# Performance work log

Hardware: AMD Instinct MI355X
Metric: run time of the kernel (lower is better)

## Reference

```python
import jax, jax.numpy as jnp
import numpy as np

H = 512      # rnn_cell_dim
CE = 128     # char_embedding
WE = 256     # word_embedding
NC = 256     # num_chars
NW = 100000  # num_words
U = 2048     # unique word forms in batch
TC = 16      # max chars per word
B = 256      # batch (sentences)
TW = 64      # max sentence length


def setup_inputs() -> dict:
    key = jax.random.key(0)
    ks = jax.random.split(key, 16)
    s = 0.05
    n = jax.random.normal
    return {
        "charseqs": jax.random.randint(ks[0], (U, TC), 0, NC),
        "charseq_lens": jax.random.randint(ks[1], (U,), 1, TC + 1),
        "charseq_ids": jax.random.randint(ks[2], (B, TW), 0, U),
        "word_ids": jax.random.randint(ks[3], (B, TW), 0, NW),
        "sentence_lens": jax.random.randint(ks[4], (B,), 1, TW + 1),
        "char_emb": n(ks[5], (NC, CE)) * s,
        "word_emb": n(ks[6], (NW, WE)) * s,
        # char GRU (shared between fw/bw, as in the TF1 code which passes the same cell)
        "Wg_c": n(ks[7], (CE + H, 2 * H)) * s,
        "bg_c": jnp.ones((2 * H,)),   # TF GRUCell gate bias init = 1.0
        "Wc_c": n(ks[8], (CE + H, H)) * s,
        "bc_c": jnp.zeros((H,)),
        # word GRU: input = concat(char bi-state 2H, word_emb WE)
        "Wg_w": n(ks[9], (2 * H + WE + H, 2 * H)) * s,
        "bg_w": jnp.ones((2 * H,)),
        "Wc_w": n(ks[10], (2 * H + WE + H, H)) * s,
        "bc_w": jnp.zeros((H,)),
        # fc head: 2H -> 64 -> 2
        "W1": n(ks[11], (2 * H, 64)) * s,
        "b1": jnp.zeros((64,)),
        "W2": n(ks[12], (64, 2)) * s,
        "b2": jnp.zeros((2,)),
    }


def _gru_final(xs, lengths, Wg, bg, Wc, bc):
    # xs: [N, T, D]; returns final state [N, H], frozen past each sequence length
    N, T, _ = xs.shape
    Hd = Wc.shape[1]
    mask = jnp.arange(T)[None, :] < lengths[:, None]  # [N, T]

    def step(h, xm):
        x, m = xm
        gates = jax.nn.sigmoid(jnp.concatenate([x, h], axis=-1) @ Wg + bg)
        r, u = jnp.split(gates, 2, axis=-1)
        c = jnp.tanh(jnp.concatenate([x, r * h], axis=-1) @ Wc + bc)
        hn = u * h + (1.0 - u) * c
        return jnp.where(m[:, None], hn, h), None

    h0 = jnp.zeros((N, Hd), xs.dtype)
    hT, _ = jax.lax.scan(step, h0, (jnp.swapaxes(xs, 0, 1), mask.T))
    return hT


def _bi_gru_final(xs, lengths, Wg, bg, Wc, bc):
    # bidirectional final states with shared weights; bw = run on per-row reversed seq
    T = xs.shape[1]
    fw = _gru_final(xs, lengths, Wg, bg, Wc, bc)
    ridx = jnp.clip(lengths[:, None] - 1 - jnp.arange(T)[None, :], 0, T - 1)  # [N, T]
    rev = jnp.take_along_axis(xs, ridx[:, :, None], axis=1)
    bw = _gru_final(rev, lengths, Wg, bg, Wc, bc)
    return jnp.concatenate([fw, bw], axis=-1)  # [N, 2H]


def reference(charseqs, charseq_lens, charseq_ids, word_ids, sentence_lens,
              char_emb, word_emb, Wg_c, bg_c, Wc_c, bc_c,
              Wg_w, bg_w, Wc_w, bc_w, W1, b1, W2, b2):
    # char embeddings + char bi-GRU over unique word forms
    input_chars = char_emb[charseqs]                                   # [U, TC, CE]
    char_states = _bi_gru_final(input_chars, charseq_lens, Wg_c, bg_c, Wc_c, bc_c)  # [U, 2H]
    input_char_words = char_states[charseq_ids]                        # [B, TW, 2H]
    # word embeddings (dropout off: inference)
    input_words = word_emb[word_ids]                                   # [B, TW, WE]
    inputs = jnp.concatenate([input_char_words, input_words], axis=2)  # [B, TW, 2H+WE]
    states = _bi_gru_final(inputs, sentence_lens, Wg_w, bg_w, Wc_w, bc_w)  # [B, 2H]
    hidden = jax.nn.leaky_relu(states @ W1 + b1, 0.2)  # tf.nn.leaky_relu alpha=0.2
    logits = hidden @ W2 + b2                                          # [B, 2]
    return logits
```

## Files before the change

### kernel.cpp

```cpp
#include <hip/hip_runtime.h>
#include <math.h>


#define TILE 64
#define BKK 16

typedef __attribute__((ext_vector_type(8))) short bshort8;
typedef __attribute__((ext_vector_type(4))) float f32x4;

enum AMode { A_PLAIN = 0, A_CHARSTATE = 1, A_RH = 2, A_GATHER = 3 };
enum EMode { E_BIAS = 0, E_GATE_CHAR = 1, E_CAND_CHAR = 2, E_XW = 3 };

struct GemmArgs {
  int M, N, K;
  const float* A; int lda;
  const float* G; int ldg;
  const int*   arows;
  const float* B;
  const float* bias;
  const float* XT; int ldxt;
  const int*   seqs;
  const int*   lens;
  int t, T;
  const int*   cidx;
  const float* Hin;
  float* Cout; int ldc;
};

__device__ __forceinline__ float sigmoidf_(float x) { return 1.0f / (1.0f + expf(-x)); }
__device__ __forceinline__ float bf2f_(unsigned short u) {
  return __uint_as_float((unsigned int)u << 16);
}
__device__ __forceinline__ unsigned short f2bf_(float f) {
  const unsigned int u = __float_as_uint(f);
  return (unsigned short)((u + 0x7FFFu + ((u >> 16) & 1u)) >> 16);
}

template<int AM, int EM>
__global__ __launch_bounds__(256) void gemm_k(GemmArgs p) {
  __shared__ float As[BKK][TILE];
  __shared__ float Bs[BKK][TILE];
  const int tid = threadIdx.x;
  const int tx = tid & 15, ty = tid >> 4;
  const int m0 = blockIdx.y * TILE, n0 = blockIdx.x * TILE;
  const int la_r = tid >> 2, la_k = (tid & 3) << 2;
  const int lb_k = tid >> 4, lb_n = (tid & 15) << 2;

  float acc[4][4] = {};
  int arow = 0;
  if constexpr (AM == A_GATHER) arow = p.arows[m0 + la_r];

  for (int k0 = 0; k0 < p.K; k0 += BKK) {
    float4 av;
    const int m = m0 + la_r;
    const int k = k0 + la_k;
    if constexpr (AM == A_PLAIN) {
      av = *reinterpret_cast<const float4*>(p.A + (size_t)m * p.lda + k);
    } else if constexpr (AM == A_CHARSTATE) {
      const float* ap = (k < 512) ? (p.A + (size_t)m * 512 + k)
                                  : (p.A + (size_t)(2048 + m) * 512 + (k - 512));
      av = *reinterpret_cast<const float4*>(ap);
    } else {
      av = *reinterpret_cast<const float4*>(p.A + (size_t)arow * p.lda + k);
    }
    As[la_k + 0][la_r] = av.x;
    As[la_k + 1][la_r] = av.y;
    As[la_k + 2][la_r] = av.z;
    As[la_k + 3][la_r] = av.w;
    float4 bv = *reinterpret_cast<const float4*>(p.B + (size_t)(k0 + lb_k) * p.N + n0 + lb_n);
    *reinterpret_cast<float4*>(&Bs[lb_k][lb_n]) = bv;
    __syncthreads();
#pragma unroll
    for (int kk = 0; kk < BKK; ++kk) {
      float4 a = *reinterpret_cast<const float4*>(&As[kk][ty << 2]);
      float4 b = *reinterpret_cast<const float4*>(&Bs[kk][tx << 2]);
      acc[0][0] += a.x * b.x; acc[0][1] += a.x * b.y; acc[0][2] += a.x * b.z; acc[0][3] += a.x * b.w;
      acc[1][0] += a.y * b.x; acc[1][1] += a.y * b.y; acc[1][2] += a.y * b.z; acc[1][3] += a.y * b.w;
      acc[2][0] += a.z * b.x; acc[2][1] += a.z * b.y; acc[2][2] += a.z * b.z; acc[2][3] += a.z * b.w;
      acc[3][0] += a.w * b.x; acc[3][1] += a.w * b.y; acc[3][2] += a.w * b.z; acc[3][3] += a.w * b.w;
    }
    __syncthreads();
  }

  const int rbase = m0 + (ty << 2);
  const int cbase = n0 + (tx << 2);
#pragma unroll
  for (int i = 0; i < 4; ++i) {
    const int row = rbase + i;
    if constexpr (EM == E_BIAS) {
#pragma unroll
      for (int j = 0; j < 4; ++j) {
        const int col = cbase + j;
        p.Cout[(size_t)row * p.ldc + col] = acc[i][j] + p.bias[col];
      }
    } else {
      const int cs = p.cidx[row];
      const float* xrow = p.XT + (size_t)cs * p.ldxt;
#pragma unroll
      for (int j = 0; j < 4; ++j) {
        const int col = cbase + j;
        p.Cout[(size_t)row * p.ldc + col] = acc[i][j] + xrow[col];
      }
    }
  }
}

__global__ __launch_bounds__(256) void wconv_k(const float* __restrict__ src,
                                               unsigned short* __restrict__ dst,
                                               int n) {
  const int i = blockIdx.x * 256 + threadIdx.x;
  if (i < n) dst[i] = f2bf_(src[i]);
}

template<int BN, int EM>
__global__ __launch_bounds__(256) void cgemm_mfma(
    const float* __restrict__ Ain,
    const float* __restrict__ G,
    const unsigned short* __restrict__ Bw,
    int ldb,
    const float* __restrict__ XT,
    const int* __restrict__ seqs,
    const int* __restrict__ lens,
    int t,
    const float* __restrict__ Hin,
    float* __restrict__ Cout, int ldc) {
  __shared__ unsigned short As[64][40];
  __shared__ unsigned short Bs[BN][40];
  __shared__ int xo_s[64];
  __shared__ int msk_s[64];

  const int tid = threadIdx.x;
  const int m0 = blockIdx.y * 64;
  const int n0 = blockIdx.x * BN;

  if (tid < 64) {
    const int grow = m0 + tid;
    const int us = grow & 2047;
    const bool dir = grow >= 2048;
    const int len = lens[us];
    int pos = dir ? (len - 1 - t) : t;
    pos = pos < 0 ? 0 : (pos > 15 ? 15 : pos);
    const int ch = seqs[us * 16 + pos];
    xo_s[tid] = ch * ((EM == 0) ? 1024 : 512);
    msk_s[tid] = (t < len) ? 1 : 0;
  }

  const int wid = tid >> 6, lane = tid & 63;
  const int lr = lane & 15, lk = (lane >> 4) << 3;
  constexpr int NI = BN / 64;
  const int c0w = wid * (BN / 4);

  f32x4 acc[4][NI];
#pragma unroll
  for (int mi = 0; mi < 4; ++mi)
#pragma unroll
    for (int ni = 0; ni < NI; ++ni) acc[mi][ni] = (f32x4){0.f, 0.f, 0.f, 0.f};

  const int arow = tid >> 2;
  const int akoff = (tid & 3) << 3;

  for (int k0 = 0; k0 < 512; k0 += 32) {
    {
      const float* ap = Ain + (size_t)(m0 + arow) * 512 + k0 + akoff;
      float4 a0 = *reinterpret_cast<const float4*>(ap);
      float4 a1 = *reinterpret_cast<const float4*>(ap + 4);
      if constexpr (EM == 1) {
        const float* gp = G + (size_t)(m0 + arow) * 1024 + k0 + akoff;
        float4 g0 = *reinterpret_cast<const float4*>(gp);
        float4 g1 = *reinterpret_cast<const float4*>(gp + 4);
        a0.x *= g0.x; a0.y *= g0.y; a0.z *= g0.z; a0.w *= g0.w;
        a1.x *= g1.x; a1.y *= g1.y; a1.z *= g1.z; a1.w *= g1.w;
      }
      bshort8 av;
      av[0] = (short)f2bf_(a0.x); av[1] = (short)f2bf_(a0.y);
      av[2] = (short)f2bf_(a0.z); av[3] = (short)f2bf_(a0.w);
      av[4] = (short)f2bf_(a1.x); av[5] = (short)f2bf_(a1.y);
      av[6] = (short)f2bf_(a1.z); av[7] = (short)f2bf_(a1.w);
      *reinterpret_cast<bshort8*>(&As[arow][akoff]) = av;
    }
    if (BN == 128 || tid < 128) {
      const int bc0 = (BN == 128) ? ((tid & 31) << 2) : ((tid & 15) << 2);
      const int bk0 = (BN == 128) ? ((tid >> 5) << 2) : ((tid >> 4) << 2);
      ushort4 b0 = *reinterpret_cast<const ushort4*>(Bw + (size_t)(k0 + bk0 + 0) * ldb + n0 + bc0);
      ushort4 b1 = *reinterpret_cast<const ushort4*>(Bw + (size_t)(k0 + bk0 + 1) * ldb + n0 + bc0);
      ushort4 b2 = *reinterpret_cast<const ushort4*>(Bw + (size_t)(k0 + bk0 + 2) * ldb + n0 + bc0);
      ushort4 b3 = *reinterpret_cast<const ushort4*>(Bw + (size_t)(k0 + bk0 + 3) * ldb + n0 + bc0);
      ushort4 w;
      w.x = b0.x; w.y = b1.x; w.z = b2.x; w.w = b3.x;
      *reinterpret_cast<ushort4*>(&Bs[bc0 + 0][bk0]) = w;
      w.x = b0.y; w.y = b1.y; w.z = b2.y; w.w = b3.y;
      *reinterpret_cast<ushort4*>(&Bs[bc0 + 1][bk0]) = w;
      w.x = b0.z; w.y = b1.z; w.z = b2.z; w.w = b3.z;
      *reinterpret_cast<ushort4*>(&Bs[bc0 + 2][bk0]) = w;
      w.x = b0.w; w.y = b1.w; w.z = b2.w; w.w = b3.w;
      *reinterpret_cast<ushort4*>(&Bs[bc0 + 3][bk0]) = w;
    }
    __syncthreads();

    bshort8 af[4];
#pragma unroll
    for (int mi = 0; mi < 4; ++mi)
      af[mi] = *reinterpret_cast<const bshort8*>(&As[mi * 16 + lr][lk]);
#pragma unroll
    for (int ni = 0; ni < NI; ++ni) {
      const bshort8 bf = *reinterpret_cast<const bshort8*>(&Bs[c0w + ni * 16 + lr][lk]);
#pragma unroll
      for (int mi = 0; mi < 4; ++mi)
        acc[mi][ni] = __builtin_amdgcn_mfma_f32_16x16x32_bf16(af[mi], bf, acc[mi][ni], 0, 0, 0);
    }
    __syncthreads();
  }

  const int rq = lane >> 4;
#pragma unroll
  for (int mi = 0; mi < 4; ++mi) {
#pragma unroll
    for (int ni = 0; ni < NI; ++ni) {
#pragma unroll
      for (int reg = 0; reg < 4; ++reg) {
        const int lrow = mi * 16 + rq * 4 + reg;
        const int grow = m0 + lrow;
        const int col = n0 + c0w + ni * 16 + lr;
        const float v = acc[mi][ni][reg];
        if constexpr (EM == 0) {
          Cout[(size_t)grow * ldc + col] = sigmoidf_(v + XT[xo_s[lrow] + col]);
        } else {
          const float cv = tanhf(v + XT[xo_s[lrow] + col]);
          const float u = G[(size_t)grow * 1024 + 512 + col];
          const float h = Hin[(size_t)grow * 512 + col];
          Cout[(size_t)grow * ldc + col] = msk_s[lrow] ? (u * h + (1.0f - u) * cv) : h;
        }
      }
    }
  }
}

template<int R, int NU, int TT>
__global__ __launch_bounds__(256) void gru_word_bf(
    const unsigned short* __restrict__ Whg,
    const unsigned short* __restrict__ Whc,
    const float* __restrict__ Xg,
    const float* __restrict__ Xc,
    const int*   __restrict__ lens,
    float* __restrict__ Hout)
{
  __shared__ float h_s [R][512];
  __shared__ float rh_s[R][512];
  __shared__ float u_s [R][512];
  __shared__ int   xog_s[R];
  __shared__ int   xoc_s[R];
  __shared__ int   msk_s[R];

  const int tid  = threadIdx.x;
  const int row0 = blockIdx.x * R;
  const int us0  = row0 & (NU - 1);
  const bool bw  = row0 >= NU;

  for (int i = tid; i < R * 512; i += 256) h_s[i >> 9][i & 511] = 0.0f;
  int mylen = 0;
  if (tid < R) mylen = lens[us0 + tid];
  __syncthreads();

  const int c0 = tid << 2;
  const int c2 = tid << 1;

  for (int t = 0; t < TT; ++t) {
    if (tid < R) {
      int pos = bw ? (mylen - 1 - t) : t;
      pos = pos < 0 ? 0 : (pos > TT - 1 ? TT - 1 : pos);
      const int xr = (us0 + tid) * TT + pos;
      xog_s[tid] = xr * 1024;
      xoc_s[tid] = xr * 512;
      msk_s[tid] = (t < mylen) ? 1 : 0;
    }
    __syncthreads();

    float4 acc[R];
#pragma unroll
    for (int r = 0; r < R; ++r) acc[r] = make_float4(0.f, 0.f, 0.f, 0.f);
#pragma unroll 2
    for (int k0 = 0; k0 < 512; k0 += 4) {
      ushort4 wu[4];
#pragma unroll
      for (int i = 0; i < 4; ++i)
        wu[i] = *reinterpret_cast<const ushort4*>(Whg + (size_t)(k0 + i) * 1024 + c0);
      float4 hv[R];
#pragma unroll
      for (int r = 0; r < R; ++r)
        hv[r] = *reinterpret_cast<const float4*>(&h_s[r][k0]);
#pragma unroll
      for (int i = 0; i < 4; ++i) {
        const float wx = bf2f_(wu[i].x), wy = bf2f_(wu[i].y);
        const float wz = bf2f_(wu[i].z), ww = bf2f_(wu[i].w);
#pragma unroll
        for (int r = 0; r < R; ++r) {
          const float h = (i == 0) ? hv[r].x : (i == 1) ? hv[r].y : (i == 2) ? hv[r].z : hv[r].w;
          acc[r].x += h * wx; acc[r].y += h * wy;
          acc[r].z += h * wz; acc[r].w += h * ww;
        }
      }
    }
#pragma unroll
    for (int r = 0; r < R; ++r) {
      const float4 x = *reinterpret_cast<const float4*>(Xg + xog_s[r] + c0);
      float4 g;
      g.x = sigmoidf_(acc[r].x + x.x);
      g.y = sigmoidf_(acc[r].y + x.y);
      g.z = sigmoidf_(acc[r].z + x.z);
      g.w = sigmoidf_(acc[r].w + x.w);
      if (c0 < 512) {
        const float4 hh = *reinterpret_cast<const float4*>(&h_s[r][c0]);
        rh_s[r][c0 + 0] = g.x * hh.x;
        rh_s[r][c0 + 1] = g.y * hh.y;
        rh_s[r][c0 + 2] = g.z * hh.z;
        rh_s[r][c0 + 3] = g.w * hh.w;
      } else {
        u_s[r][c0 - 512 + 0] = g.x;
        u_s[r][c0 - 512 + 1] = g.y;
        u_s[r][c0 - 512 + 2] = g.z;
        u_s[r][c0 - 512 + 3] = g.w;
      }
    }
    __syncthreads();

    float2 acc2[R];
#pragma unroll
    for (int r = 0; r < R; ++r) acc2[r] = make_float2(0.f, 0.f);
#pragma unroll 2
    for (int k0 = 0; k0 < 512; k0 += 4) {
      ushort2 wu[4];
#pragma unroll
      for (int i = 0; i < 4; ++i)
        wu[i] = *reinterpret_cast<const ushort2*>(Whc + (size_t)(k0 + i) * 512 + c2);
      float4 rv[R];
#pragma unroll
      for (int r = 0; r < R; ++r)
        rv[r] = *reinterpret_cast<const float4*>(&rh_s[r][k0]);
#pragma unroll
      for (int i = 0; i < 4; ++i) {
        const float wx = bf2f_(wu[i].x), wy = bf2f_(wu[i].y);
#pragma unroll
        for (int r = 0; r < R; ++r) {
          const float rvv = (i == 0) ? rv[r].x : (i == 1) ? rv[r].y : (i == 2) ? rv[r].z : rv[r].w;
          acc2[r].x += rvv * wx; acc2[r].y += rvv * wy;
        }
      }
    }
#pragma unroll
    for (int r = 0; r < R; ++r) {
      const float2 x = *reinterpret_cast<const float2*>(Xc + xoc_s[r] + c2);
      const float cx = tanhf(acc2[r].x + x.x);
      const float cy = tanhf(acc2[r].y + x.y);
      if (msk_s[r]) {
        const float ux = u_s[r][c2], uy = u_s[r][c2 + 1];
        const float hx = h_s[r][c2], hy = h_s[r][c2 + 1];
        h_s[r][c2]     = ux * hx + (1.0f - ux) * cx;
        h_s[r][c2 + 1] = uy * hy + (1.0f - uy) * cy;
      }
    }
    __syncthreads();
  }

  for (int i = tid; i < R * 512; i += 256)
    Hout[(size_t)(row0 + (i >> 9)) * 512 + (i & 511)] = h_s[i >> 9][i & 511];
}

__global__ __launch_bounds__(64) void head_k(const float* __restrict__ Hw,
                                             const float* __restrict__ W1,
                                             const float* __restrict__ b1,
                                             const float* __restrict__ W2,
                                             const float* __restrict__ b2,
                                             float* __restrict__ out) {
  __shared__ float s[1024];
  __shared__ float hid[64];
  const int b = blockIdx.x;
  const int tid = threadIdx.x;
  for (int k = tid; k < 512; k += 64) {
    s[k]       = Hw[(size_t)b * 512 + k];
    s[512 + k] = Hw[(size_t)(256 + b) * 512 + k];
  }
  __syncthreads();
  float acc = b1[tid];
  for (int k = 0; k < 1024; ++k) acc += s[k] * W1[k * 64 + tid];
  acc = acc > 0.0f ? acc : 0.2f * acc;
  hid[tid] = acc;
  __syncthreads();
  if (tid < 2) {
    float a = b2[tid];
    for (int k = 0; k < 64; ++k) a += hid[k] * W2[k * 2 + tid];
    out[b * 2 + tid] = a;
  }
}

extern "C" void kernel_launch(void* const* d_in, const int* in_sizes, int n_in,
                              void* d_out, int out_size, void* d_ws, size_t ws_size,
                              hipStream_t stream) {
  const int*   charseqs      = (const int*)d_in[0];
  const int*   charseq_lens  = (const int*)d_in[1];
  const int*   charseq_ids   = (const int*)d_in[2];
  const int*   word_ids      = (const int*)d_in[3];
  const int*   sentence_lens = (const int*)d_in[4];
  const float* char_emb      = (const float*)d_in[5];
  const float* word_emb      = (const float*)d_in[6];
  const float* Wg_c          = (const float*)d_in[7];
  const float* bg_c          = (const float*)d_in[8];
  const float* Wc_c          = (const float*)d_in[9];
  const float* bc_c          = (const float*)d_in[10];
  const float* Wg_w          = (const float*)d_in[11];
  const float* bg_w          = (const float*)d_in[12];
  const float* Wc_w          = (const float*)d_in[13];
  const float* bc_w          = (const float*)d_in[14];
  const float* W1            = (const float*)d_in[15];
  const float* b1            = (const float*)d_in[16];
  const float* W2            = (const float*)d_in[17];
  const float* b2            = (const float*)d_in[18];
  float* out = (float*)d_out;

  float* ws = (float*)d_ws;
  size_t off = 0;
  auto alloc = [&](size_t n) { float* p = ws + off; off += n; return p; };
  float* XTABg = alloc(256 * 1024);
  float* XTABc = alloc(256 * 512);
  float* HcA   = alloc((size_t)4096 * 512);
  float* HcB   = alloc((size_t)4096 * 512);
  float* Gc    = alloc((size_t)4096 * 1024);
  float* CTABg = alloc((size_t)2048 * 1024);
  float* CTABc = alloc((size_t)2048 * 512);
  float* XWg   = alloc((size_t)16384 * 1024);
  float* XWc   = alloc((size_t)16384 * 512);
  float* Hw    = alloc(512 * 512);
  unsigned short* WhgBF = (unsigned short*)alloc(512 * 1024 / 2);
  unsigned short* WhcBF = (unsigned short*)alloc(512 * 512 / 2);
  unsigned short* WgcBF = (unsigned short*)alloc(512 * 1024 / 2);
  unsigned short* WccBF = (unsigned short*)alloc(512 * 512 / 2);

  hipMemsetAsync(HcA, 0, (size_t)4096 * 512 * sizeof(float), stream);

  wconv_k<<<(512 * 1024 + 255) / 256, 256, 0, stream>>>(
      Wg_w + (size_t)1280 * 1024, WhgBF, 512 * 1024);
  wconv_k<<<(512 * 512 + 255) / 256, 256, 0, stream>>>(
      Wc_w + (size_t)1280 * 512, WhcBF, 512 * 512);
  wconv_k<<<(512 * 1024 + 255) / 256, 256, 0, stream>>>(
      Wg_c + 128 * 1024, WgcBF, 512 * 1024);
  wconv_k<<<(512 * 512 + 255) / 256, 256, 0, stream>>>(
      Wc_c + 128 * 512, WccBF, 512 * 512);

  {
    GemmArgs a{}; a.M = 256; a.N = 1024; a.K = 128;
    a.A = char_emb; a.lda = 128; a.B = Wg_c; a.bias = bg_c; a.Cout = XTABg; a.ldc = 1024;
    gemm_k<A_PLAIN, E_BIAS><<<dim3(1024 / TILE, 256 / TILE), 256, 0, stream>>>(a);
    GemmArgs c{}; c.M = 256; c.N = 512; c.K = 128;
    c.A = char_emb; c.lda = 128; c.B = Wc_c; c.bias = bc_c; c.Cout = XTABc; c.ldc = 512;
    gemm_k<A_PLAIN, E_BIAS><<<dim3(512 / TILE, 256 / TILE), 256, 0, stream>>>(c);
  }

  float* hcur = HcA; float* hnext = HcB;
  for (int t = 0; t < 16; ++t) {
    cgemm_mfma<128, 0><<<dim3(1024 / 128, 4096 / 64), 256, 0, stream>>>(
        hcur, nullptr, WgcBF, 1024, XTABg, charseqs, charseq_lens, t, nullptr,
        Gc, 1024);
    cgemm_mfma<64, 1><<<dim3(512 / 64, 4096 / 64), 256, 0, stream>>>(
        hcur, Gc, WccBF, 512, XTABc, charseqs, charseq_lens, t, hcur,
        hnext, 512);
    float* tmp = hcur; hcur = hnext; hnext = tmp;
  }

  {
    GemmArgs a{}; a.M = 2048; a.N = 1024; a.K = 1024;
    a.A = hcur; a.B = Wg_w; a.bias = bg_w; a.Cout = CTABg; a.ldc = 1024;
    gemm_k<A_CHARSTATE, E_BIAS><<<dim3(1024 / TILE, 2048 / TILE), 256, 0, stream>>>(a);
    GemmArgs c{}; c.M = 2048; c.N = 512; c.K = 1024;
    c.A = hcur; c.B = Wc_w; c.bias = bc_w; c.Cout = CTABc; c.ldc = 512;
    gemm_k<A_CHARSTATE, E_BIAS><<<dim3(512 / TILE, 2048 / TILE), 256, 0, stream>>>(c);
  }

  {
    GemmArgs a{}; a.M = 16384; a.N = 1024; a.K = 256;
    a.A = word_emb; a.lda = 256; a.arows = word_ids; a.B = Wg_w + (size_t)1024 * 1024;
    a.XT = CTABg; a.ldxt = 1024; a.cidx = charseq_ids; a.Cout = XWg; a.ldc = 1024;
    gemm_k<A_GATHER, E_XW><<<dim3(1024 / TILE, 16384 / TILE), 256, 0, stream>>>(a);
    GemmArgs c{}; c.M = 16384; c.N = 512; c.K = 256;
    c.A = word_emb; c.lda = 256; c.arows = word_ids; c.B = Wc_w + (size_t)1024 * 512;
    c.XT = CTABc; c.ldxt = 512; c.cidx = charseq_ids; c.Cout = XWc; c.ldc = 512;
    gemm_k<A_GATHER, E_XW><<<dim3(512 / TILE, 16384 / TILE), 256, 0, stream>>>(c);
  }

  gru_word_bf<2, 256, 64><<<256, 256, 0, stream>>>(
      WhgBF, WhcBF, XWg, XWc, sentence_lens, Hw);

  head_k<<<256, 64, 0, stream>>>(Hw, W1, b1, W2, b2, out);
}
```

Before: 3.628 ms.

## Replace persistent word GRU kernel with per-timestep MFMA gemm launches

The word-level bidirectional GRU was a single persistent kernel where each block handled two rows with scalar FMAs, rereading the full bf16 recurrent weights every step. It now reuses the char-level MFMA gemm kernels (templated on a mode flag for indexing) and launches two kernels per timestep over 64 steps with ping-pong hidden buffers. This cuts redundant weight traffic and uses matrix cores, at the cost of 128 extra launches with small grids (64 blocks) and global round-trips of gate state.

```diff
diff --git a/kernel.cpp b/kernel.cpp
--- a/kernel.cpp
+++ b/kernel.cpp
@@ -112,7 +112,7 @@
   if (i < n) dst[i] = f2bf_(src[i]);
 }
 
-template<int BN, int EM>
+template<int BN, int EM, bool CHARM>
 __global__ __launch_bounds__(256) void cgemm_mfma(
     const float* __restrict__ Ain,
     const float* __restrict__ G,
@@ -135,13 +135,16 @@
 
   if (tid < 64) {
     const int grow = m0 + tid;
-    const int us = grow & 2047;
-    const bool dir = grow >= 2048;
+    const int us = grow & (CHARM ? 2047 : 255);
+    const bool dir = grow >= (CHARM ? 2048 : 256);
     const int len = lens[us];
+    constexpr int TTv = CHARM ? 16 : 64;
     int pos = dir ? (len - 1 - t) : t;
-    pos = pos < 0 ? 0 : (pos > 15 ? 15 : pos);
-    const int ch = seqs[us * 16 + pos];
-    xo_s[tid] = ch * ((EM == 0) ? 1024 : 512);
+    pos = pos < 0 ? 0 : (pos > TTv - 1 ? TTv - 1 : pos);
+    int xr;
+    if constexpr (CHARM) xr = seqs[us * 16 + pos];
+    else                 xr = us * 64 + pos;
+    xo_s[tid] = xr * ((EM == 0) ? 1024 : 512);
     msk_s[tid] = (t < len) ? 1 : 0;
   }
 
@@ -233,136 +236,6 @@
       }
     }
   }
-}
-
-template<int R, int NU, int TT>
-__global__ __launch_bounds__(256) void gru_word_bf(
-    const unsigned short* __restrict__ Whg,
-    const unsigned short* __restrict__ Whc,
-    const float* __restrict__ Xg,
-    const float* __restrict__ Xc,
-    const int*   __restrict__ lens,
-    float* __restrict__ Hout)
-{
-  __shared__ float h_s [R][512];
-  __shared__ float rh_s[R][512];
-  __shared__ float u_s [R][512];
-  __shared__ int   xog_s[R];
-  __shared__ int   xoc_s[R];
-  __shared__ int   msk_s[R];
-
-  const int tid  = threadIdx.x;
-  const int row0 = blockIdx.x * R;
-  const int us0  = row0 & (NU - 1);
-  const bool bw  = row0 >= NU;
-
-  for (int i = tid; i < R * 512; i += 256) h_s[i >> 9][i & 511] = 0.0f;
-  int mylen = 0;
-  if (tid < R) mylen = lens[us0 + tid];
-  __syncthreads();
-
-  const int c0 = tid << 2;
-  const int c2 = tid << 1;
-
-  for (int t = 0; t < TT; ++t) {
-    if (tid < R) {
-      int pos = bw ? (mylen - 1 - t) : t;
-      pos = pos < 0 ? 0 : (pos > TT - 1 ? TT - 1 : pos);
-      const int xr = (us0 + tid) * TT + pos;
-      xog_s[tid] = xr * 1024;
-      xoc_s[tid] = xr * 512;
-      msk_s[tid] = (t < mylen) ? 1 : 0;
-    }
-    __syncthreads();
-
-    float4 acc[R];
-#pragma unroll
-    for (int r = 0; r < R; ++r) acc[r] = make_float4(0.f, 0.f, 0.f, 0.f);
-#pragma unroll 2
-    for (int k0 = 0; k0 < 512; k0 += 4) {
-      ushort4 wu[4];
-#pragma unroll
-      for (int i = 0; i < 4; ++i)
-        wu[i] = *reinterpret_cast<const ushort4*>(Whg + (size_t)(k0 + i) * 1024 + c0);
-      float4 hv[R];
-#pragma unroll
-      for (int r = 0; r < R; ++r)
-        hv[r] = *reinterpret_cast<const float4*>(&h_s[r][k0]);
-#pragma unroll
-      for (int i = 0; i < 4; ++i) {
-        const float wx = bf2f_(wu[i].x), wy = bf2f_(wu[i].y);
-        const float wz = bf2f_(wu[i].z), ww = bf2f_(wu[i].w);
-#pragma unroll
-        for (int r = 0; r < R; ++r) {
-          const float h = (i == 0) ? hv[r].x : (i == 1) ? hv[r].y : (i == 2) ? hv[r].z : hv[r].w;
-          acc[r].x += h * wx; acc[r].y += h * wy;
-          acc[r].z += h * wz; acc[r].w += h * ww;
-        }
-      }
-    }
-#pragma unroll
-    for (int r = 0; r < R; ++r) {
-      const float4 x = *reinterpret_cast<const float4*>(Xg + xog_s[r] + c0);
-      float4 g;
-      g.x = sigmoidf_(acc[r].x + x.x);
-      g.y = sigmoidf_(acc[r].y + x.y);
-      g.z = sigmoidf_(acc[r].z + x.z);
-      g.w = sigmoidf_(acc[r].w + x.w);
-      if (c0 < 512) {
-        const float4 hh = *reinterpret_cast<const float4*>(&h_s[r][c0]);
-        rh_s[r][c0 + 0] = g.x * hh.x;
-        rh_s[r][c0 + 1] = g.y * hh.y;
-        rh_s[r][c0 + 2] = g.z * hh.z;
-        rh_s[r][c0 + 3] = g.w * hh.w;
-      } else {
-        u_s[r][c0 - 512 + 0] = g.x;
-        u_s[r][c0 - 512 + 1] = g.y;
-        u_s[r][c0 - 512 + 2] = g.z;
-        u_s[r][c0 - 512 + 3] = g.w;
-      }
-    }
-    __syncthreads();
-
-    float2 acc2[R];
-#pragma unroll
-    for (int r = 0; r < R; ++r) acc2[r] = make_float2(0.f, 0.f);
-#pragma unroll 2
-    for (int k0 = 0; k0 < 512; k0 += 4) {
-      ushort2 wu[4];
-#pragma unroll
-      for (int i = 0; i < 4; ++i)
-        wu[i] = *reinterpret_cast<const ushort2*>(Whc + (size_t)(k0 + i) * 512 + c2);
-      float4 rv[R];
-#pragma unroll
-      for (int r = 0; r < R; ++r)
-        rv[r] = *reinterpret_cast<const float4*>(&rh_s[r][k0]);
-#pragma unroll
-      for (int i = 0; i < 4; ++i) {
-        const float wx = bf2f_(wu[i].x), wy = bf2f_(wu[i].y);
-#pragma unroll
-        for (int r = 0; r < R; ++r) {
-          const float rvv = (i == 0) ? rv[r].x : (i == 1) ? rv[r].y : (i == 2) ? rv[r].z : rv[r].w;
-          acc2[r].x += rvv * wx; acc2[r].y += rvv * wy;
-        }
-      }
-    }
-#pragma unroll
-    for (int r = 0; r < R; ++r) {
-      const float2 x = *reinterpret_cast<const float2*>(Xc + xoc_s[r] + c2);
-      const float cx = tanhf(acc2[r].x + x.x);
-      const float cy = tanhf(acc2[r].y + x.y);
-      if (msk_s[r]) {
-        const float ux = u_s[r][c2], uy = u_s[r][c2 + 1];
-        const float hx = h_s[r][c2], hy = h_s[r][c2 + 1];
-        h_s[r][c2]     = ux * hx + (1.0f - ux) * cx;
-        h_s[r][c2 + 1] = uy * hy + (1.0f - uy) * cy;
-      }
-    }
-    __syncthreads();
-  }
-
-  for (int i = tid; i < R * 512; i += 256)
-    Hout[(size_t)(row0 + (i >> 9)) * 512 + (i & 511)] = h_s[i >> 9][i & 511];
 }
 
 __global__ __launch_bounds__(64) void head_k(const float* __restrict__ Hw,
@@ -428,13 +301,16 @@
   float* CTABc = alloc((size_t)2048 * 512);
   float* XWg   = alloc((size_t)16384 * 1024);
   float* XWc   = alloc((size_t)16384 * 512);
-  float* Hw    = alloc(512 * 512);
+  float* HwA   = alloc(512 * 512);
+  float* HwB   = alloc(512 * 512);
+  float* Gw    = alloc((size_t)512 * 1024);
   unsigned short* WhgBF = (unsigned short*)alloc(512 * 1024 / 2);
   unsigned short* WhcBF = (unsigned short*)alloc(512 * 512 / 2);
   unsigned short* WgcBF = (unsigned short*)alloc(512 * 1024 / 2);
   unsigned short* WccBF = (unsigned short*)alloc(512 * 512 / 2);
 
   hipMemsetAsync(HcA, 0, (size_t)4096 * 512 * sizeof(float), stream);
+  hipMemsetAsync(HwA, 0, (size_t)512 * 512 * sizeof(float), stream);
 
   wconv_k<<<(512 * 1024 + 255) / 256, 256, 0, stream>>>(
       Wg_w + (size_t)1280 * 1024, WhgBF, 512 * 1024);
@@ -456,10 +332,10 @@
 
   float* hcur = HcA; float* hnext = HcB;
   for (int t = 0; t < 16; ++t) {
-    cgemm_mfma<128, 0><<<dim3(1024 / 128, 4096 / 64), 256, 0, stream>>>(
+    cgemm_mfma<128, 0, true><<<dim3(1024 / 128, 4096 / 64), 256, 0, stream>>>(
         hcur, nullptr, WgcBF, 1024, XTABg, charseqs, charseq_lens, t, nullptr,
         Gc, 1024);
-    cgemm_mfma<64, 1><<<dim3(512 / 64, 4096 / 64), 256, 0, stream>>>(
+    cgemm_mfma<64, 1, true><<<dim3(512 / 64, 4096 / 64), 256, 0, stream>>>(
         hcur, Gc, WccBF, 512, XTABc, charseqs, charseq_lens, t, hcur,
         hnext, 512);
     float* tmp = hcur; hcur = hnext; hnext = tmp;
@@ -485,8 +361,16 @@
     gemm_k<A_GATHER, E_XW><<<dim3(512 / TILE, 16384 / TILE), 256, 0, stream>>>(c);
   }
 
-  gru_word_bf<2, 256, 64><<<256, 256, 0, stream>>>(
-      WhgBF, WhcBF, XWg, XWc, sentence_lens, Hw);
-
-  head_k<<<256, 64, 0, stream>>>(Hw, W1, b1, W2, b2, out);
-}
+  float* wcur = HwA; float* wnext = HwB;
+  for (int t = 0; t < 64; ++t) {
+    cgemm_mfma<128, 0, false><<<dim3(1024 / 128, 512 / 64), 256, 0, stream>>>(
+        wcur, nullptr, WhgBF, 1024, XWg, nullptr, sentence_lens, t, nullptr,
+        Gw, 1024);
+    cgemm_mfma<64, 1, false><<<dim3(512 / 64, 512 / 64), 256, 0, stream>>>(
+        wcur, Gw, WhcBF, 512, XWc, nullptr, sentence_lens, t, wcur,
+        wnext, 512);
+    float* tmp = wcur; wcur = wnext; wnext = tmp;
+  }
+
+  head_k<<<256, 64, 0, stream>>>(wcur, W1, b1, W2, b2, out);
+}
```

Result: slower. 4.362 ms (+20.2%).

## Pack word-GRU recurrent weights per thread and double block threads

Applied to the files above, without the earlier changes.

Repacks the word-GRU recurrent weights into a per-thread contiguous bf16 layout, so each thread reads its column slice for eight k values with one 16-byte load. The kernel now runs 512 threads per block, each owning 2 gate columns and 1 candidate column. This is meant to cut per-step recurrent latency by giving the GRU more parallel threads and wider weight loads. In exchange, one thread's consecutive loads walk a contiguous stream while neighbouring threads sit 2 KB apart, so accesses within a warp are no longer coalesced. Register pressure per thread also changes.

```diff
diff --git a/kernel.cpp b/kernel.cpp
--- a/kernel.cpp
+++ b/kernel.cpp
@@ -110,6 +110,21 @@
                                                int n) {
   const int i = blockIdx.x * 256 + threadIdx.x;
   if (i < n) dst[i] = f2bf_(src[i]);
+}
+
+template<int CPT>
+__global__ __launch_bounds__(256) void wpack_k(const float* __restrict__ src,
+                                               unsigned short* __restrict__ dst,
+                                               int ldb) {
+  const int i = blockIdx.x * 256 + threadIdx.x;
+  const int n = 512 * ldb;
+  if (i < n) {
+    const int t = i / (512 * CPT);
+    const int rem = i - t * (512 * CPT);
+    const int k = rem / CPT;
+    const int j = rem - k * CPT;
+    dst[i] = f2bf_(src[(size_t)k * ldb + t * CPT + j]);
+  }
 }
 
 template<int BN, int EM>
@@ -236,9 +251,9 @@
 }
 
 template<int R, int NU, int TT>
-__global__ __launch_bounds__(256) void gru_word_bf(
-    const unsigned short* __restrict__ Whg,
-    const unsigned short* __restrict__ Whc,
+__global__ __launch_bounds__(512) void gru_word_bf(
+    const unsigned short* __restrict__ WPg,
+    const unsigned short* __restrict__ WPc,
     const float* __restrict__ Xg,
     const float* __restrict__ Xc,
     const int*   __restrict__ lens,
@@ -256,13 +271,15 @@
   const int us0  = row0 & (NU - 1);
   const bool bw  = row0 >= NU;
 
-  for (int i = tid; i < R * 512; i += 256) h_s[i >> 9][i & 511] = 0.0f;
+  for (int i = tid; i < R * 512; i += 512) h_s[i >> 9][i & 511] = 0.0f;
   int mylen = 0;
   if (tid < R) mylen = lens[us0 + tid];
   __syncthreads();
 
-  const int c0 = tid << 2;
-  const int c2 = tid << 1;
+  const int cg = tid << 1;
+  const int cc = tid;
+  const unsigned short* wpg = WPg + (size_t)tid * 1024;
+  const unsigned short* wpc = WPc + (size_t)tid * 512;
 
   for (int t = 0; t < TT; ++t) {
     if (tid < R) {
@@ -275,93 +292,80 @@
     }
     __syncthreads();
 
-    float4 acc[R];
-#pragma unroll
-    for (int r = 0; r < R; ++r) acc[r] = make_float4(0.f, 0.f, 0.f, 0.f);
-#pragma unroll 2
+    float2 acc[R];
+#pragma unroll
+    for (int r = 0; r < R; ++r) acc[r] = make_float2(0.f, 0.f);
+#pragma unroll 4
     for (int k0 = 0; k0 < 512; k0 += 4) {
-      ushort4 wu[4];
-#pragma unroll
-      for (int i = 0; i < 4; ++i)
-        wu[i] = *reinterpret_cast<const ushort4*>(Whg + (size_t)(k0 + i) * 1024 + c0);
+      const bshort8 w = *reinterpret_cast<const bshort8*>(wpg + k0 * 2);
       float4 hv[R];
 #pragma unroll
       for (int r = 0; r < R; ++r)
         hv[r] = *reinterpret_cast<const float4*>(&h_s[r][k0]);
 #pragma unroll
       for (int i = 0; i < 4; ++i) {
-        const float wx = bf2f_(wu[i].x), wy = bf2f_(wu[i].y);
-        const float wz = bf2f_(wu[i].z), ww = bf2f_(wu[i].w);
+        const float wx = bf2f_((unsigned short)w[2 * i]);
+        const float wy = bf2f_((unsigned short)w[2 * i + 1]);
 #pragma unroll
         for (int r = 0; r < R; ++r) {
-          const float h = (i == 0) ? hv[r].x : (i == 1) ? hv[r].y : (i == 2) ? hv[r].z : hv[r].w;
-          acc[r].x += h * wx; acc[r].y += h * wy;
-          acc[r].z += h * wz; acc[r].w += h * ww;
+          const float hval = (i == 0) ? hv[r].x : (i == 1) ? hv[r].y : (i == 2) ? hv[r].z : hv[r].w;
+          acc[r].x += hval * wx; acc[r].y += hval * wy;
         }
       }
     }
 #pragma unroll
     for (int r = 0; r < R; ++r) {
-      const float4 x = *reinterpret_cast<const float4*>(Xg + xog_s[r] + c0);
-      float4 g;
+      const float2 x = *reinterpret_cast<const float2*>(Xg + xog_s[r] + cg);
+      float2 g;
       g.x = sigmoidf_(acc[r].x + x.x);
       g.y = sigmoidf_(acc[r].y + x.y);
-      g.z = sigmoidf_(acc[r].z + x.z);
-      g.w = sigmoidf_(acc[r].w + x.w);
-      if (c0 < 512) {
-        const float4 hh = *reinterpret_cast<const float4*>(&h_s[r][c0]);
-        rh_s[r][c0 + 0] = g.x * hh.x;
-        rh_s[r][c0 + 1] = g.y * hh.y;
-        rh_s[r][c0 + 2] = g.z * hh.z;
-        rh_s[r][c0 + 3] = g.w * hh.w;
+      if (cg < 512) {
+        rh_s[r][cg + 0] = g.x * h_s[r][cg + 0];
+        rh_s[r][cg + 1] = g.y * h_s[r][cg + 1];
       } else {
-        u_s[r][c0 - 512 + 0] = g.x;
-        u_s[r][c0 - 512 + 1] = g.y;
-        u_s[r][c0 - 512 + 2] = g.z;
-        u_s[r][c0 - 512 + 3] = g.w;
-      }
-    }
-    __syncthreads();
-
-    float2 acc2[R];
-#pragma unroll
-    for (int r = 0; r < R; ++r) acc2[r] = make_float2(0.f, 0.f);
-#pragma unroll 2
-    for (int k0 = 0; k0 < 512; k0 += 4) {
-      ushort2 wu[4];
-#pragma unroll
-      for (int i = 0; i < 4; ++i)
-        wu[i] = *reinterpret_cast<const ushort2*>(Whc + (size_t)(k0 + i) * 512 + c2);
-      float4 rv[R];
-#pragma unroll
-      for (int r = 0; r < R; ++r)
-        rv[r] = *reinterpret_cast<const float4*>(&rh_s[r][k0]);
-#pragma unroll
-      for (int i = 0; i < 4; ++i) {
-        const float wx = bf2f_(wu[i].x), wy = bf2f_(wu[i].y);
+        u_s[r][cg - 512 + 0] = g.x;
+        u_s[r][cg - 512 + 1] = g.y;
+      }
+    }
+    __syncthreads();
+
+    float acc2[R];
+#pragma unroll
+    for (int r = 0; r < R; ++r) acc2[r] = 0.f;
+#pragma unroll 4
+    for (int k0 = 0; k0 < 512; k0 += 8) {
+      const bshort8 w = *reinterpret_cast<const bshort8*>(wpc + k0);
+      float4 r0[R], r1[R];
+#pragma unroll
+      for (int r = 0; r < R; ++r) {
+        r0[r] = *reinterpret_cast<const float4*>(&rh_s[r][k0]);
+        r1[r] = *reinterpret_cast<const float4*>(&rh_s[r][k0 + 4]);
+      }
+#pragma unroll
+      for (int i = 0; i < 8; ++i) {
+        const float wv = bf2f_((unsigned short)w[i]);
 #pragma unroll
         for (int r = 0; r < R; ++r) {
-          const float rvv = (i == 0) ? rv[r].x : (i == 1) ? rv[r].y : (i == 2) ? rv[r].z : rv[r].w;
-          acc2[r].x += rvv * wx; acc2[r].y += rvv * wy;
+          const float rv = (i == 0) ? r0[r].x : (i == 1) ? r0[r].y : (i == 2) ? r0[r].z :
+                           (i == 3) ? r0[r].w : (i == 4) ? r1[r].x : (i == 5) ? r1[r].y :
+                           (i == 6) ? r1[r].z : r1[r].w;
+          acc2[r] += rv * wv;
         }
       }
     }
 #pragma unroll
     for (int r = 0; r < R; ++r) {
-      const float2 x = *reinterpret_cast<const float2*>(Xc + xoc_s[r] + c2);
-      const float cx = tanhf(acc2[r].x + x.x);
-      const float cy = tanhf(acc2[r].y + x.y);
+      const float cv = tanhf(acc2[r] + Xc[xoc_s[r] + cc]);
       if (msk_s[r]) {
-        const float ux = u_s[r][c2], uy = u_s[r][c2 + 1];
-        const float hx = h_s[r][c2], hy = h_s[r][c2 + 1];
-        h_s[r][c2]     = ux * hx + (1.0f - ux) * cx;
-        h_s[r][c2 + 1] = uy * hy + (1.0f - uy) * cy;
-      }
-    }
-    __syncthreads();
-  }
-
-  for (int i = tid; i < R * 512; i += 256)
+        const float u = u_s[r][cc];
+        const float h = h_s[r][cc];
+        h_s[r][cc] = u * h + (1.0f - u) * cv;
+      }
+    }
+    __syncthreads();
+  }
+
+  for (int i = tid; i < R * 512; i += 512)
     Hout[(size_t)(row0 + (i >> 9)) * 512 + (i & 511)] = h_s[i >> 9][i & 511];
 }
 
@@ -429,17 +433,17 @@
   float* XWg   = alloc((size_t)16384 * 1024);
   float* XWc   = alloc((size_t)16384 * 512);
   float* Hw    = alloc(512 * 512);
-  unsigned short* WhgBF = (unsigned short*)alloc(512 * 1024 / 2);
-  unsigned short* WhcBF = (unsigned short*)alloc(512 * 512 / 2);
+  unsigned short* WPg   = (unsigned short*)alloc(512 * 1024 / 2);
+  unsigned short* WPc   = (unsigned short*)alloc(512 * 512 / 2);
   unsigned short* WgcBF = (unsigned short*)alloc(512 * 1024 / 2);
   unsigned short* WccBF = (unsigned short*)alloc(512 * 512 / 2);
 
   hipMemsetAsync(HcA, 0, (size_t)4096 * 512 * sizeof(float), stream);
 
-  wconv_k<<<(512 * 1024 + 255) / 256, 256, 0, stream>>>(
-      Wg_w + (size_t)1280 * 1024, WhgBF, 512 * 1024);
-  wconv_k<<<(512 * 512 + 255) / 256, 256, 0, stream>>>(
-      Wc_w + (size_t)1280 * 512, WhcBF, 512 * 512);
+  wpack_k<2><<<(512 * 1024 + 255) / 256, 256, 0, stream>>>(
+      Wg_w + (size_t)1280 * 1024, WPg, 1024);
+  wpack_k<1><<<(512 * 512 + 255) / 256, 256, 0, stream>>>(
+      Wc_w + (size_t)1280 * 512, WPc, 512);
   wconv_k<<<(512 * 1024 + 255) / 256, 256, 0, stream>>>(
       Wg_c + 128 * 1024, WgcBF, 512 * 1024);
   wconv_k<<<(512 * 512 + 255) / 256, 256, 0, stream>>>(
@@ -485,8 +489,8 @@
     gemm_k<A_GATHER, E_XW><<<dim3(512 / TILE, 16384 / TILE), 256, 0, stream>>>(c);
   }
 
-  gru_word_bf<2, 256, 64><<<256, 256, 0, stream>>>(
-      WhgBF, WhcBF, XWg, XWc, sentence_lens, Hw);
+  gru_word_bf<2, 256, 64><<<256, 512, 0, stream>>>(
+      WPg, WPc, XWg, XWc, sentence_lens, Hw);
 
   head_k<<<256, 64, 0, stream>>>(Hw, W1, b1, W2, b2, out);
 }
```

New measurement: 7.270 ms. +100.4%, slower.

## Move word-embedding gather GEMMs to bf16 MFMA kernel and keep per-row indices in registers

Applied to the files above, without the earlier changes.

The two large gathered word-embedding projections (16384x256 into 1024 and 512 columns), previously computed by a scalar fp32 tiled GEMM, now run on the bf16 MFMA kernel. That kernel gains gather-row and charstate-index modes, and two extra weight slices are converted to bf16. The word GRU kernel now computes per-row offsets and masks in registers instead of shared memory, which removes one barrier per timestep. The trade-off is reduced precision in the word input projection, plus a few extra conversion launches.

```diff
diff --git a/kernel.cpp b/kernel.cpp
--- a/kernel.cpp
+++ b/kernel.cpp
@@ -8,22 +8,14 @@
 typedef __attribute__((ext_vector_type(8))) short bshort8;
 typedef __attribute__((ext_vector_type(4))) float f32x4;
 
-enum AMode { A_PLAIN = 0, A_CHARSTATE = 1, A_RH = 2, A_GATHER = 3 };
-enum EMode { E_BIAS = 0, E_GATE_CHAR = 1, E_CAND_CHAR = 2, E_XW = 3 };
+enum AMode { A_PLAIN = 0, A_CHARSTATE = 1 };
+enum EMode { E_BIAS = 0 };
 
 struct GemmArgs {
   int M, N, K;
   const float* A; int lda;
-  const float* G; int ldg;
-  const int*   arows;
   const float* B;
   const float* bias;
-  const float* XT; int ldxt;
-  const int*   seqs;
-  const int*   lens;
-  int t, T;
-  const int*   cidx;
-  const float* Hin;
   float* Cout; int ldc;
 };
 
@@ -47,8 +39,6 @@
   const int lb_k = tid >> 4, lb_n = (tid & 15) << 2;
 
   float acc[4][4] = {};
-  int arow = 0;
-  if constexpr (AM == A_GATHER) arow = p.arows[m0 + la_r];
 
   for (int k0 = 0; k0 < p.K; k0 += BKK) {
     float4 av;
@@ -56,12 +46,10 @@
     const int k = k0 + la_k;
     if constexpr (AM == A_PLAIN) {
       av = *reinterpret_cast<const float4*>(p.A + (size_t)m * p.lda + k);
-    } else if constexpr (AM == A_CHARSTATE) {
+    } else {
       const float* ap = (k < 512) ? (p.A + (size_t)m * 512 + k)
                                   : (p.A + (size_t)(2048 + m) * 512 + (k - 512));
       av = *reinterpret_cast<const float4*>(ap);
-    } else {
-      av = *reinterpret_cast<const float4*>(p.A + (size_t)arow * p.lda + k);
     }
     As[la_k + 0][la_r] = av.x;
     As[la_k + 1][la_r] = av.y;
@@ -87,20 +75,10 @@
 #pragma unroll
   for (int i = 0; i < 4; ++i) {
     const int row = rbase + i;
-    if constexpr (EM == E_BIAS) {
-#pragma unroll
-      for (int j = 0; j < 4; ++j) {
-        const int col = cbase + j;
-        p.Cout[(size_t)row * p.ldc + col] = acc[i][j] + p.bias[col];
-      }
-    } else {
-      const int cs = p.cidx[row];
-      const float* xrow = p.XT + (size_t)cs * p.ldxt;
-#pragma unroll
-      for (int j = 0; j < 4; ++j) {
-        const int col = cbase + j;
-        p.Cout[(size_t)row * p.ldc + col] = acc[i][j] + xrow[col];
-      }
+#pragma unroll
+    for (int j = 0; j < 4; ++j) {
+      const int col = cbase + j;
+      p.Cout[(size_t)row * p.ldc + col] = acc[i][j] + p.bias[col];
     }
   }
 }
@@ -112,16 +90,18 @@
   if (i < n) dst[i] = f2bf_(src[i]);
 }
 
-template<int BN, int EM>
+template<int BN, int AM, int EM>
 __global__ __launch_bounds__(256) void cgemm_mfma(
-    const float* __restrict__ Ain,
+    const float* __restrict__ Ain, int lda,
     const float* __restrict__ G,
     const unsigned short* __restrict__ Bw,
-    int ldb,
-    const float* __restrict__ XT,
+    int ldb, int K,
+    const float* __restrict__ XT, int ldxt,
     const int* __restrict__ seqs,
     const int* __restrict__ lens,
     int t,
+    const int* __restrict__ arows,
+    const int* __restrict__ cidx,
     const float* __restrict__ Hin,
     float* __restrict__ Cout, int ldc) {
   __shared__ unsigned short As[64][40];
@@ -135,14 +115,19 @@
 
   if (tid < 64) {
     const int grow = m0 + tid;
-    const int us = grow & 2047;
-    const bool dir = grow >= 2048;
-    const int len = lens[us];
-    int pos = dir ? (len - 1 - t) : t;
-    pos = pos < 0 ? 0 : (pos > 15 ? 15 : pos);
-    const int ch = seqs[us * 16 + pos];
-    xo_s[tid] = ch * ((EM == 0) ? 1024 : 512);
-    msk_s[tid] = (t < len) ? 1 : 0;
+    if constexpr (EM == 2) {
+      xo_s[tid] = cidx[grow] * ldxt;
+      msk_s[tid] = 1;
+    } else {
+      const int us = grow & 2047;
+      const bool dir = grow >= 2048;
+      const int len = lens[us];
+      int pos = dir ? (len - 1 - t) : t;
+      pos = pos < 0 ? 0 : (pos > 15 ? 15 : pos);
+      const int ch = seqs[us * 16 + pos];
+      xo_s[tid] = ch * ldxt;
+      msk_s[tid] = (t < len) ? 1 : 0;
+    }
   }
 
   const int wid = tid >> 6, lane = tid & 63;
@@ -158,13 +143,15 @@
 
   const int arow = tid >> 2;
   const int akoff = (tid & 3) << 3;
-
-  for (int k0 = 0; k0 < 512; k0 += 32) {
+  int agrow = m0 + arow;
+  if constexpr (AM == 2) agrow = arows[m0 + arow];
+
+  for (int k0 = 0; k0 < K; k0 += 32) {
     {
-      const float* ap = Ain + (size_t)(m0 + arow) * 512 + k0 + akoff;
+      const float* ap = Ain + (size_t)agrow * lda + k0 + akoff;
       float4 a0 = *reinterpret_cast<const float4*>(ap);
       float4 a1 = *reinterpret_cast<const float4*>(ap + 4);
-      if constexpr (EM == 1) {
+      if constexpr (AM == 1) {
         const float* gp = G + (size_t)(m0 + arow) * 1024 + k0 + akoff;
         float4 g0 = *reinterpret_cast<const float4*>(gp);
         float4 g1 = *reinterpret_cast<const float4*>(gp + 4);
@@ -224,11 +211,13 @@
         const float v = acc[mi][ni][reg];
         if constexpr (EM == 0) {
           Cout[(size_t)grow * ldc + col] = sigmoidf_(v + XT[xo_s[lrow] + col]);
-        } else {
+        } else if constexpr (EM == 1) {
           const float cv = tanhf(v + XT[xo_s[lrow] + col]);
           const float u = G[(size_t)grow * 1024 + 512 + col];
           const float h = Hin[(size_t)grow * 512 + col];
           Cout[(size_t)grow * ldc + col] = msk_s[lrow] ? (u * h + (1.0f - u) * cv) : h;
+        } else {
+          Cout[(size_t)grow * ldc + col] = v + XT[xo_s[lrow] + col];
         }
       }
     }
@@ -247,9 +236,6 @@
   __shared__ float h_s [R][512];
   __shared__ float rh_s[R][512];
   __shared__ float u_s [R][512];
-  __shared__ int   xog_s[R];
-  __shared__ int   xoc_s[R];
-  __shared__ int   msk_s[R];
 
   const int tid  = threadIdx.x;
   const int row0 = blockIdx.x * R;
@@ -257,23 +243,25 @@
   const bool bw  = row0 >= NU;
 
   for (int i = tid; i < R * 512; i += 256) h_s[i >> 9][i & 511] = 0.0f;
-  int mylen = 0;
-  if (tid < R) mylen = lens[us0 + tid];
+  int lenr[R];
+#pragma unroll
+  for (int r = 0; r < R; ++r) lenr[r] = lens[us0 + r];
   __syncthreads();
 
   const int c0 = tid << 2;
   const int c2 = tid << 1;
 
   for (int t = 0; t < TT; ++t) {
-    if (tid < R) {
-      int pos = bw ? (mylen - 1 - t) : t;
+    int xog[R], xoc[R], msk[R];
+#pragma unroll
+    for (int r = 0; r < R; ++r) {
+      int pos = bw ? (lenr[r] - 1 - t) : t;
       pos = pos < 0 ? 0 : (pos > TT - 1 ? TT - 1 : pos);
-      const int xr = (us0 + tid) * TT + pos;
-      xog_s[tid] = xr * 1024;
-      xoc_s[tid] = xr * 512;
-      msk_s[tid] = (t < mylen) ? 1 : 0;
-    }
-    __syncthreads();
+      const int xr = (us0 + r) * TT + pos;
+      xog[r] = xr * 1024;
+      xoc[r] = xr * 512;
+      msk[r] = (t < lenr[r]) ? 1 : 0;
+    }
 
     float4 acc[R];
 #pragma unroll
@@ -302,7 +290,7 @@
     }
 #pragma unroll
     for (int r = 0; r < R; ++r) {
-      const float4 x = *reinterpret_cast<const float4*>(Xg + xog_s[r] + c0);
+      const float4 x = *reinterpret_cast<const float4*>(Xg + xog[r] + c0);
       float4 g;
       g.x = sigmoidf_(acc[r].x + x.x);
       g.y = sigmoidf_(acc[r].y + x.y);
@@ -348,10 +336,10 @@
     }
 #pragma unroll
     for (int r = 0; r < R; ++r) {
-      const float2 x = *reinterpret_cast<const float2*>(Xc + xoc_s[r] + c2);
+      const float2 x = *reinterpret_cast<const float2*>(Xc + xoc[r] + c2);
       const float cx = tanhf(acc2[r].x + x.x);
       const float cy = tanhf(acc2[r].y + x.y);
-      if (msk_s[r]) {
+      if (msk[r]) {
         const float ux = u_s[r][c2], uy = u_s[r][c2 + 1];
         const float hx = h_s[r][c2], hy = h_s[r][c2 + 1];
         h_s[r][c2]     = ux * hx + (1.0f - ux) * cx;
@@ -433,6 +421,8 @@
   unsigned short* WhcBF = (unsigned short*)alloc(512 * 512 / 2);
   unsigned short* WgcBF = (unsigned short*)alloc(512 * 1024 / 2);
   unsigned short* WccBF = (unsigned short*)alloc(512 * 512 / 2);
+  unsigned short* WgwBF = (unsigned short*)alloc(256 * 1024 / 2);
+  unsigned short* WcwBF = (unsigned short*)alloc(256 * 512 / 2);
 
   hipMemsetAsync(HcA, 0, (size_t)4096 * 512 * sizeof(float), stream);
 
@@ -444,6 +434,10 @@
       Wg_c + 128 * 1024, WgcBF, 512 * 1024);
   wconv_k<<<(512 * 512 + 255) / 256, 256, 0, stream>>>(
       Wc_c + 128 * 512, WccBF, 512 * 512);
+  wconv_k<<<(256 * 1024 + 255) / 256, 256, 0, stream>>>(
+      Wg_w + (size_t)1024 * 1024, WgwBF, 256 * 1024);
+  wconv_k<<<(256 * 512 + 255) / 256, 256, 0, stream>>>(
+      Wc_w + (size_t)1024 * 512, WcwBF, 256 * 512);
 
   {
     GemmArgs a{}; a.M = 256; a.N = 1024; a.K = 128;
@@ -456,12 +450,12 @@
 
   float* hcur = HcA; float* hnext = HcB;
   for (int t = 0; t < 16; ++t) {
-    cgemm_mfma<128, 0><<<dim3(1024 / 128, 4096 / 64), 256, 0, stream>>>(
-        hcur, nullptr, WgcBF, 1024, XTABg, charseqs, charseq_lens, t, nullptr,
-        Gc, 1024);
-    cgemm_mfma<64, 1><<<dim3(512 / 64, 4096 / 64), 256, 0, stream>>>(
-        hcur, Gc, WccBF, 512, XTABc, charseqs, charseq_lens, t, hcur,
-        hnext, 512);
+    cgemm_mfma<128, 0, 0><<<dim3(1024 / 128, 4096 / 64), 256, 0, stream>>>(
+        hcur, 512, nullptr, WgcBF, 1024, 512, XTABg, 1024,
+        charseqs, charseq_lens, t, nullptr, nullptr, nullptr, Gc, 1024);
+    cgemm_mfma<64, 1, 1><<<dim3(512 / 64, 4096 / 64), 256, 0, stream>>>(
+        hcur, 512, Gc, WccBF, 512, 512, XTABc, 512,
+        charseqs, charseq_lens, t, nullptr, nullptr, hcur, hnext, 512);
     float* tmp = hcur; hcur = hnext; hnext = tmp;
   }
 
@@ -475,14 +469,12 @@
   }
 
   {
-    GemmArgs a{}; a.M = 16384; a.N = 1024; a.K = 256;
-    a.A = word_emb; a.lda = 256; a.arows = word_ids; a.B = Wg_w + (size_t)1024 * 1024;
-    a.XT = CTABg; a.ldxt = 1024; a.cidx = charseq_ids; a.Cout = XWg; a.ldc = 1024;
-    gemm_k<A_GATHER, E_XW><<<dim3(1024 / TILE, 16384 / TILE), 256, 0, stream>>>(a);
-    GemmArgs c{}; c.M = 16384; c.N = 512; c.K = 256;
-    c.A = word_emb; c.lda = 256; c.arows = word_ids; c.B = Wc_w + (size_t)1024 * 512;
-    c.XT = CTABc; c.ldxt = 512; c.cidx = charseq_ids; c.Cout = XWc; c.ldc = 512;
-    gemm_k<A_GATHER, E_XW><<<dim3(512 / TILE, 16384 / TILE), 256, 0, stream>>>(c);
+    cgemm_mfma<128, 2, 2><<<dim3(1024 / 128, 16384 / 64), 256, 0, stream>>>(
+        word_emb, 256, nullptr, WgwBF, 1024, 256, CTABg, 1024,
+        nullptr, nullptr, 0, word_ids, charseq_ids, nullptr, XWg, 1024);
+    cgemm_mfma<64, 2, 2><<<dim3(512 / 64, 16384 / 64), 256, 0, stream>>>(
+        word_emb, 256, nullptr, WcwBF, 512, 256, CTABc, 512,
+        nullptr, nullptr, 0, word_ids, charseq_ids, nullptr, XWc, 512);
   }
 
   gru_word_bf<2, 256, 64><<<256, 256, 0, stream>>>(
```

Result: faster. 3.497 ms (-3.6%).
